# Kernel tuning notes

Hardware: AMD Instinct MI355X
Metric: run time of the kernel (lower is better)

The kernel has to match this reference:

```python
import jax, jax.numpy as jnp
import numpy as np

GAMMA = 0.99
LMBDA = 0.95
B, T = 8192, 2048


def setup_inputs() -> dict:
    key = jax.random.key(0)
    k1, k2, k3, k4 = jax.random.split(key, 4)
    reward = jax.random.normal(k1, (B, T), dtype=jnp.float32)
    terminated = jax.random.randint(k2, (B, T), 0, 2, dtype=jnp.int32)
    value = jax.random.normal(k3, (B, T), dtype=jnp.float32)
    next_value = jax.random.normal(k4, (B, T), dtype=jnp.float32)
    return {"reward": reward, "terminated": terminated, "value": value, "next_value": next_value}


def reference(reward, terminated, value, next_value):
    # not_done: [B, T]
    not_done = 1.0 - terminated.astype(jnp.float32)
    # delta_t = r_t + gamma * V(s_{t+1}) * nd_t - V(s_t)   (all elementwise, [B, T])
    delta = reward + GAMMA * next_value * not_done - value
    gl = GAMMA * LMBDA

    # backward recurrence over time: gae_t = delta_t + gamma*lmbda*nd_t*gae_{t+1}
    def step(gae, xs):  # gae: [B]
        d_t, nd_t = xs  # each [B]
        gae = d_t + gl * nd_t * gae
        return gae, gae

    xs = (jnp.swapaxes(delta, 0, 1), jnp.swapaxes(not_done, 0, 1))  # [T, B]
    init = jnp.zeros((reward.shape[0],), dtype=reward.dtype)
    _, adv_tb = jax.lax.scan(step, init, xs, reverse=True)  # [T, B], time-ordered
    advantages = jnp.swapaxes(adv_tb, 0, 1)  # [B, T]
    returns = advantages + value
    return advantages, returns
```

## Files before the change

kernel.cpp:

```cpp
#include <hip/hip_runtime.h>


constexpr float GAMMA_F = 0.99f;
constexpr float GL      = 0.99f * 0.95f;
constexpr int   T_LEN   = 2048;
constexpr int   CHUNK   = 32;
constexpr int   WAVES_PER_BLOCK = 4;

constexpr float gl_pow32() {
    double p = 1.0;
    for (int i = 0; i < 32; ++i) p *= (double)GL;
    return (float)p;
}
constexpr float GL32 = gl_pow32();

__global__ __launch_bounds__(256)
void gae_kernel(const float* __restrict__ reward,
                const int*   __restrict__ term,
                const float* __restrict__ value,
                const float* __restrict__ next_value,
                float* __restrict__ adv_out,
                float* __restrict__ ret_out,
                int rows) {
    const int wid  = threadIdx.x >> 6;
    const int lane = threadIdx.x & 63;
    const int row  = blockIdx.x * WAVES_PER_BLOCK + wid;
    if (row >= rows) return;

    const long base = (long)row * T_LEN + lane * CHUNK;

    const float4* r4 = reinterpret_cast<const float4*>(reward + base);
    const int4*   t4 = reinterpret_cast<const int4*>(term + base);
    const float4* v4 = reinterpret_cast<const float4*>(value + base);
    const float4* n4 = reinterpret_cast<const float4*>(next_value + base);

    float d[CHUNK];
    float val[CHUNK];
    unsigned mask = 0;

#pragma unroll
    for (int k = 0; k < CHUNK / 4; ++k) {
        float4 r  = r4[k];
        int4   tm = t4[k];
        float4 v  = v4[k];
        float4 nv = n4[k];
        float rr[4] = {r.x, r.y, r.z, r.w};
        int   tt[4] = {tm.x, tm.y, tm.z, tm.w};
        float vv[4] = {v.x, v.y, v.z, v.w};
        float nn[4] = {nv.x, nv.y, nv.z, nv.w};
#pragma unroll
        for (int j = 0; j < 4; ++j) {
            const int i = 4 * k + j;
            const float nd = (float)(1 - tt[j]);
            d[i]   = fmaf(GAMMA_F * nd, nn[j], rr[j]) - vv[j];
            val[i] = vv[j];
            mask  |= (tt[j] ? 0u : 1u) << i;
        }
    }

    float g = 0.0f;
#pragma unroll
    for (int i = CHUNK - 1; i >= 0; --i) {
        const float c = ((mask >> i) & 1u) ? GL : 0.0f;
        g = fmaf(c, g, d[i]);
    }
    float A  = (mask == 0xFFFFFFFFu) ? GL32 : 0.0f;
    float Bc = g;

#pragma unroll
    for (int off = 1; off < 64; off <<= 1) {
        const float A2 = __shfl_down(A, off, 64);
        const float B2 = __shfl_down(Bc, off, 64);
        if (lane + off < 64) {
            Bc = fmaf(A, B2, Bc);
            A *= A2;
        }
    }
    float gin = __shfl_down(Bc, 1, 64);
    if (lane == 63) gin = 0.0f;

    float4* a4 = reinterpret_cast<float4*>(adv_out + base);
    float4* o4 = reinterpret_cast<float4*>(ret_out + base);
    g = gin;
#pragma unroll
    for (int k = CHUNK / 4 - 1; k >= 0; --k) {
        float ga[4], ra[4];
#pragma unroll
        for (int j = 3; j >= 0; --j) {
            const int i = 4 * k + j;
            const float c = ((mask >> i) & 1u) ? GL : 0.0f;
            g = fmaf(c, g, d[i]);
            ga[j] = g;
            ra[j] = g + val[i];
        }
        a4[k] = make_float4(ga[0], ga[1], ga[2], ga[3]);
        o4[k] = make_float4(ra[0], ra[1], ra[2], ra[3]);
    }
}

extern "C" void kernel_launch(void* const* d_in, const int* in_sizes, int n_in,
                              void* d_out, int out_size, void* d_ws, size_t ws_size,
                              hipStream_t stream) {
    const float* reward     = (const float*)d_in[0];
    const int*   terminated = (const int*)d_in[1];
    const float* value      = (const float*)d_in[2];
    const float* next_value = (const float*)d_in[3];

    const int total = in_sizes[0];
    const int rows  = total / T_LEN;

    float* adv = (float*)d_out;
    float* ret = adv + (long)total;

    const int block = 64 * WAVES_PER_BLOCK;
    const int grid  = (rows + WAVES_PER_BLOCK - 1) / WAVES_PER_BLOCK;
    gae_kernel<<<grid, block, 0, stream>>>(reward, terminated, value, next_value,
                                           adv, ret, rows);
}
```

Before: 344.1 us.

## Process each row in 512-element segments with software-prefetched loads and nontemporal stores

Each wave now walks its row backward in four 512-element segments instead of one 32-per-lane chunk. It carries the GAE state across segments and prefetches the next segment's inputs while computing the current one. Loads become contiguous 32-byte accesses per lane, which coalesce better than 128-byte strided chunks, and register pressure drops. Outputs use nontemporal stores to avoid polluting cache. The cost is four wave-level scans per row instead of one, plus a serial dependency between segments.

```diff
diff --git a/kernel.cpp b/kernel.cpp
--- a/kernel.cpp
+++ b/kernel.cpp
@@ -4,15 +4,44 @@
 constexpr float GAMMA_F = 0.99f;
 constexpr float GL      = 0.99f * 0.95f;
 constexpr int   T_LEN   = 2048;
-constexpr int   CHUNK   = 32;
-constexpr int   WAVES_PER_BLOCK = 4;
+constexpr int   PER_LANE = 8;
+constexpr int   SEG     = 64 * PER_LANE;
+constexpr int   NBLK    = T_LEN / SEG;
+constexpr int   WPB     = 4;
 
-constexpr float gl_pow32() {
+typedef float  vf4 __attribute__((ext_vector_type(4)));
+
+constexpr float gl_pow8() {
     double p = 1.0;
-    for (int i = 0; i < 32; ++i) p *= (double)GL;
+    for (int i = 0; i < 8; ++i) p *= (double)GL;
     return (float)p;
 }
-constexpr float GL32 = gl_pow32();
+constexpr float GL8 = gl_pow8();
+
+struct Raw {
+    float4 r0, r1, v0, v1, n0, n1;
+    int4   t0, t1;
+};
+
+__device__ inline Raw load_blk(const float* __restrict__ r, const int* __restrict__ t,
+                               const float* __restrict__ v, const float* __restrict__ n,
+                               long base) {
+    Raw x;
+    const float4* r4 = reinterpret_cast<const float4*>(r + base);
+    const int4*   t4 = reinterpret_cast<const int4*>(t + base);
+    const float4* v4 = reinterpret_cast<const float4*>(v + base);
+    const float4* n4 = reinterpret_cast<const float4*>(n + base);
+    x.r0 = r4[0]; x.r1 = r4[1];
+    x.t0 = t4[0]; x.t1 = t4[1];
+    x.v0 = v4[0]; x.v1 = v4[1];
+    x.n0 = n4[0]; x.n1 = n4[1];
+    return x;
+}
+
+__device__ inline void st_nt4(float* p, float a, float b, float c, float d) {
+    vf4 val = {a, b, c, d};
+    __builtin_nontemporal_store(val, reinterpret_cast<vf4*>(p));
+}
 
 __global__ __launch_bounds__(256)
 void gae_kernel(const float* __restrict__ reward,
@@ -24,77 +53,81 @@
                 int rows) {
     const int wid  = threadIdx.x >> 6;
     const int lane = threadIdx.x & 63;
-    const int row  = blockIdx.x * WAVES_PER_BLOCK + wid;
+    const int row  = blockIdx.x * WPB + wid;
     if (row >= rows) return;
 
-    const long base = (long)row * T_LEN + lane * CHUNK;
+    const long rowbase = (long)row * T_LEN;
 
-    const float4* r4 = reinterpret_cast<const float4*>(reward + base);
-    const int4*   t4 = reinterpret_cast<const int4*>(term + base);
-    const float4* v4 = reinterpret_cast<const float4*>(value + base);
-    const float4* n4 = reinterpret_cast<const float4*>(next_value + base);
-
-    float d[CHUNK];
-    float val[CHUNK];
-    unsigned mask = 0;
+    Raw cur = load_blk(reward, term, value, next_value,
+                       rowbase + (long)(NBLK - 1) * SEG + lane * PER_LANE);
+    float g_carry = 0.0f;
 
 #pragma unroll
-    for (int k = 0; k < CHUNK / 4; ++k) {
-        float4 r  = r4[k];
-        int4   tm = t4[k];
-        float4 v  = v4[k];
-        float4 nv = n4[k];
-        float rr[4] = {r.x, r.y, r.z, r.w};
-        int   tt[4] = {tm.x, tm.y, tm.z, tm.w};
-        float vv[4] = {v.x, v.y, v.z, v.w};
-        float nn[4] = {nv.x, nv.y, nv.z, nv.w};
+    for (int c = NBLK - 1; c >= 0; --c) {
+        Raw nxt;
+        if (c > 0)
+            nxt = load_blk(reward, term, value, next_value,
+                           rowbase + (long)(c - 1) * SEG + lane * PER_LANE);
+
+        float rr[8] = {cur.r0.x, cur.r0.y, cur.r0.z, cur.r0.w,
+                       cur.r1.x, cur.r1.y, cur.r1.z, cur.r1.w};
+        int   tt[8] = {cur.t0.x, cur.t0.y, cur.t0.z, cur.t0.w,
+                       cur.t1.x, cur.t1.y, cur.t1.z, cur.t1.w};
+        float vv[8] = {cur.v0.x, cur.v0.y, cur.v0.z, cur.v0.w,
+                       cur.v1.x, cur.v1.y, cur.v1.z, cur.v1.w};
+        float nn[8] = {cur.n0.x, cur.n0.y, cur.n0.z, cur.n0.w,
+                       cur.n1.x, cur.n1.y, cur.n1.z, cur.n1.w};
+        float d[8];
+        unsigned mask = 0;
 #pragma unroll
-        for (int j = 0; j < 4; ++j) {
-            const int i = 4 * k + j;
+        for (int j = 0; j < 8; ++j) {
             const float nd = (float)(1 - tt[j]);
-            d[i]   = fmaf(GAMMA_F * nd, nn[j], rr[j]) - vv[j];
-            val[i] = vv[j];
-            mask  |= (tt[j] ? 0u : 1u) << i;
+            d[j]  = fmaf(GAMMA_F * nd, nn[j], rr[j]) - vv[j];
+            mask |= (tt[j] ? 0u : 1u) << j;
         }
-    }
 
-    float g = 0.0f;
+        float Bc = 0.0f;
 #pragma unroll
-    for (int i = CHUNK - 1; i >= 0; --i) {
-        const float c = ((mask >> i) & 1u) ? GL : 0.0f;
-        g = fmaf(c, g, d[i]);
-    }
-    float A  = (mask == 0xFFFFFFFFu) ? GL32 : 0.0f;
-    float Bc = g;
+        for (int j = PER_LANE - 1; j >= 0; --j) {
+            const float a = ((mask >> j) & 1u) ? GL : 0.0f;
+            Bc = fmaf(a, Bc, d[j]);
+        }
+        float A = (mask == 0xFFu) ? GL8 : 0.0f;
 
 #pragma unroll
-    for (int off = 1; off < 64; off <<= 1) {
-        const float A2 = __shfl_down(A, off, 64);
-        const float B2 = __shfl_down(Bc, off, 64);
-        if (lane + off < 64) {
-            Bc = fmaf(A, B2, Bc);
-            A *= A2;
+        for (int off = 1; off < 64; off <<= 1) {
+            const float A2 = __shfl_down(A, off, 64);
+            const float B2 = __shfl_down(Bc, off, 64);
+            if (lane + off < 64) {
+                Bc = fmaf(A, B2, Bc);
+                A *= A2;
+            }
         }
-    }
-    float gin = __shfl_down(Bc, 1, 64);
-    if (lane == 63) gin = 0.0f;
 
-    float4* a4 = reinterpret_cast<float4*>(adv_out + base);
-    float4* o4 = reinterpret_cast<float4*>(ret_out + base);
-    g = gin;
+        const float As1 = __shfl_down(A, 1, 64);
+        const float Bs1 = __shfl_down(Bc, 1, 64);
+        const float gin = (lane == 63) ? g_carry : fmaf(As1, g_carry, Bs1);
+
+        const float A0 = __shfl(A, 0, 64);
+        const float B0 = __shfl(Bc, 0, 64);
+
+        float g = gin;
+        float ga[8], ro[8];
 #pragma unroll
-    for (int k = CHUNK / 4 - 1; k >= 0; --k) {
-        float ga[4], ra[4];
-#pragma unroll
-        for (int j = 3; j >= 0; --j) {
-            const int i = 4 * k + j;
-            const float c = ((mask >> i) & 1u) ? GL : 0.0f;
-            g = fmaf(c, g, d[i]);
+        for (int j = PER_LANE - 1; j >= 0; --j) {
+            const float a = ((mask >> j) & 1u) ? GL : 0.0f;
+            g = fmaf(a, g, d[j]);
             ga[j] = g;
-            ra[j] = g + val[i];
+            ro[j] = g + vv[j];
         }
-        a4[k] = make_float4(ga[0], ga[1], ga[2], ga[3]);
-        o4[k] = make_float4(ra[0], ra[1], ra[2], ra[3]);
+        const long ob = rowbase + (long)c * SEG + lane * PER_LANE;
+        st_nt4(adv_out + ob,     ga[0], ga[1], ga[2], ga[3]);
+        st_nt4(adv_out + ob + 4, ga[4], ga[5], ga[6], ga[7]);
+        st_nt4(ret_out + ob,     ro[0], ro[1], ro[2], ro[3]);
+        st_nt4(ret_out + ob + 4, ro[4], ro[5], ro[6], ro[7]);
+
+        g_carry = fmaf(A0, g_carry, B0);
+        if (c > 0) cur = nxt;
     }
 }
 
@@ -112,8 +145,8 @@
     float* adv = (float*)d_out;
     float* ret = adv + (long)total;
 
-    const int block = 64 * WAVES_PER_BLOCK;
-    const int grid  = (rows + WAVES_PER_BLOCK - 1) / WAVES_PER_BLOCK;
+    const int block = 64 * WPB;
+    const int grid  = (rows + WPB - 1) / WPB;
     gae_kernel<<<grid, block, 0, stream>>>(reward, terminated, value, next_value,
                                            adv, ret, rows);
 }
```

New measurement: 343.5 us. About the same (-0.2%).
